# Kernel optimization log

Hardware: AMD Instinct MI355X
Metric: run time of the kernel (lower is better)

## Reference

```python
import jax, jax.numpy as jnp
import numpy as np

# --- module hyperparameters (from init_kwargs) ---
NUM_CHANNELS = 31
WINDOW_SIZE = 3
IN_DIM = 2 * WINDOW_SIZE + 1          # 7
GRID_SIZE = 5
SPLINE_ORDER = 3
GRID_RANGE = (-1.0, 1.0)
N_BASIS = GRID_SIZE + SPLINE_ORDER    # 8 spline coefficients per input dim
COEF_LEN = IN_DIM * 1 * N_BASIS       # 56
KAN_PARAMS = COEF_LEN + IN_DIM + IN_DIM  # 70 = coef + univariate_w + residual_w


def bspline_basis(x):
    """Cox-de Boor B-spline bases of order SPLINE_ORDER on a uniform grid.
    x: [...,] -> returns [..., N_BASIS]."""
    lo, hi = GRID_RANGE
    h = (hi - lo) / GRID_SIZE
    # extended knot vector: grid_size + 2*k + 1 knots
    knots = lo + h * jnp.arange(-SPLINE_ORDER, GRID_SIZE + SPLINE_ORDER + 1,
                                dtype=x.dtype)
    xe = x[..., None]
    b = ((xe >= knots[:-1]) & (xe < knots[1:])).astype(x.dtype)
    for p in range(1, SPLINE_ORDER + 1):
        left = (xe - knots[: -(p + 1)]) / (knots[p:-1] - knots[: -(p + 1)]) * b[..., :-1]
        right = (knots[p + 1:] - xe) / (knots[p + 1:] - knots[1:-p]) * b[..., 1:]
        b = left + right
    return b  # [..., N_BASIS]


def setup_inputs() -> dict:
    key = jax.random.key(0)
    k1, k2, k3 = jax.random.split(key, 3)
    B, C, D, H, W = 2, NUM_CHANNELS, IN_DIM, 192, 192
    windowed_x = jax.random.normal(k1, (B, C, D, H, W), dtype=jnp.float32)
    # hypernetwork generator: 3x3 conv  C -> KAN_PARAMS
    gen_w = jax.random.normal(k2, (KAN_PARAMS, C, 3, 3), dtype=jnp.float32) * 0.05
    gen_b = jax.random.normal(k3, (KAN_PARAMS,), dtype=jnp.float32) * 0.05
    return {"windowed_x": windowed_x, "gen_w": gen_w, "gen_b": gen_b}


def reference(windowed_x, gen_w, gen_b):
    B, C, D, H, W = windowed_x.shape
    # shared-params branch: global context -> per-pixel KAN weights
    ctx = windowed_x.mean(axis=2)  # [B, C, H, W]
    wts = jax.lax.conv_general_dilated(
        ctx, gen_w, window_strides=(1, 1), padding="SAME",
        dimension_numbers=("NCHW", "OIHW", "NCHW"))
    wts = wts + gen_b[None, :, None, None]            # [B, P, H, W]
    wts = jnp.moveaxis(wts, 1, -1)                    # [B, H, W, P]
    # unpack per-pixel KAN parameters (out_dim == 1 squeezed)
    coef = wts[..., :COEF_LEN].reshape(B, H, W, D, N_BASIS)   # [B,H,W,7,8]
    uw = wts[..., COEF_LEN:COEF_LEN + D]                      # [B,H,W,7]
    rw = wts[..., COEF_LEN + D:COEF_LEN + 2 * D]              # [B,H,W,7]
    # per-pixel, per-channel spline window evaluation (weights shared over C)
    x = jnp.moveaxis(windowed_x, 2, -1)               # [B, C, H, W, 7]
    basis = bspline_basis(x)                          # [B, C, H, W, 7, 8]
    spline = jnp.einsum("bchwdg,bhwdg,bhwd->bchw", basis, coef, uw)
    resid = jnp.einsum("bchwd,bhwd->bchw", jax.nn.silu(x), rw)
    return spline + resid                             # [B, C, H, W]
```

## Files before the change

### kernel.cpp

```cpp
#include <hip/hip_runtime.h>
#include <math.h>

#define NBATCH 2
#define NC 31
#define ND 7
#define NH 192
#define NW 192
#define HW (NH * NW)
#define NP (NBATCH * HW)
#define NBASIS 8
#define CLEN 56
#define KP 70

#define N4 (NBATCH * NC * (HW / 4))
#define GWB_N (9 * 80 * 32)

#define A_WORDS (9 * 80 * 32)
#define B_WORDS (3 * 66 * 32)

#define KPX 64

typedef __attribute__((ext_vector_type(8))) short s16x8;
typedef __attribute__((ext_vector_type(4))) float f32x4;

__device__ __forceinline__ unsigned short f2bf(float f)
{
    unsigned u = __float_as_uint(f);
    u += 0x7FFFu + ((u >> 16) & 1u);
    return (unsigned short)(u >> 16);
}

__global__ __launch_bounds__(256) void ctx_mean_kernel(
    const float4* __restrict__ x4, float4* __restrict__ ctx4,
    const float* __restrict__ gw, unsigned short* __restrict__ gwb)
{
    const int HW4 = HW / 4;
    int idx = blockIdx.x * 256 + threadIdx.x;
    if (idx < N4) {
        int hw4 = idx % HW4;
        int bc  = idx / HW4;
        const float4* src = x4 + (size_t)bc * (ND * HW4) + hw4;
        float4 a = src[0];
#pragma unroll
        for (int d = 1; d < ND; ++d) {
            float4 v = src[d * HW4];
            a.x += v.x; a.y += v.y; a.z += v.z; a.w += v.w;
        }
        const float inv = 1.0f / 7.0f;
        a.x *= inv; a.y *= inv; a.z *= inv; a.w *= inv;
        ctx4[idx] = a;
        return;
    }
    int e = idx - N4;
    if (e < GWB_N) {
        int s  = e / 2560;
        int r  = e - s * 2560;
        int m  = r >> 5;
        int ic = r & 31;
        float v = (m < KP && ic < NC) ? gw[m * (NC * 9) + ic * 9 + s] : 0.f;
        gwb[e] = f2bf(v);
    }
}

__global__ __launch_bounds__(256) void conv_kernel(
    const float* __restrict__ ctx, const unsigned short* __restrict__ gwb,
    const float* __restrict__ gb, float* __restrict__ wts)
{
    __shared__ __align__(16) unsigned short AB[A_WORDS + B_WORDS];

    const int tid  = threadIdx.x;
    const int lane = tid & 63;
    const int wv   = tid >> 6;
    const int gr   = blockIdx.x / 3;
    const int x0   = (blockIdx.x % 3) * 64;
    const int b    = gr / NH;
    const int y    = gr - b * NH;

    {
        const uint4* gs = (const uint4*)gwb;
        uint4*       gd = (uint4*)AB;
        for (int f = tid; f < A_WORDS / 8; f += 256) gd[f] = gs[f];
    }

    if (tid < 3 * 66) {
        int row = tid / 66;
        int col = tid - row * 66;
        int gy = y + row - 1, gx = x0 + col - 1;
        bool ok = (gy >= 0) && (gy < NH) && (gx >= 0) && (gx < NW);
        int cgy = ok ? gy : 0, cgx = ok ? gx : 0;
        const float* src = ctx + (size_t)(b * NC) * HW + cgy * NW + cgx;
        unsigned dw[16];
        if (ok) {
            float v[NC];
#pragma unroll
            for (int ic = 0; ic < NC; ++ic) v[ic] = src[(size_t)ic * HW];
#pragma unroll
            for (int j = 0; j < 16; ++j) {
                unsigned lo = f2bf(v[2 * j]);
                unsigned hi = (2 * j + 1 < NC) ? (unsigned)f2bf(v[2 * j + 1]) : 0u;
                dw[j] = lo | (hi << 16);
            }
        } else {
#pragma unroll
            for (int j = 0; j < 16; ++j) dw[j] = 0u;
        }
        uint4* dst = (uint4*)(AB + A_WORDS + tid * 32);
#pragma unroll
        for (int q = 0; q < 4; ++q)
            dst[q] = make_uint4(dw[4 * q], dw[4 * q + 1], dw[4 * q + 2], dw[4 * q + 3]);
    }
    __syncthreads();

    const int lm = lane & 15;
    const int kb = lane >> 4;

    f32x4 acc[5];
#pragma unroll
    for (int mt = 0; mt < 5; ++mt)
#pragma unroll
        for (int j = 0; j < 4; ++j) {
            int m = mt * 16 + kb * 4 + j;
            acc[mt][j] = (m < KP) ? gb[m] : 0.f;
        }

    const unsigned short* ap = AB + lm * 32 + kb * 8;
    const unsigned short* bp = AB + A_WORDS + (wv * 16 + lm) * 32 + kb * 8;

#pragma unroll
    for (int s = 0; s < 9; ++s) {
        const int dy = s / 3, dx = s % 3;
        s16x8 bf = *(const s16x8*)(bp + (dy * 66 + dx) * 32);
#pragma unroll
        for (int mt = 0; mt < 5; ++mt) {
            s16x8 af = *(const s16x8*)(ap + (s * 80 + mt * 16) * 32);
            acc[mt] = __builtin_amdgcn_mfma_f32_16x16x32_bf16(af, bf, acc[mt], 0, 0, 0);
        }
    }

    const int p = blockIdx.x * 64 + wv * 16 + lm;
#pragma unroll
    for (int mt = 0; mt < 5; ++mt)
#pragma unroll
        for (int j = 0; j < 4; ++j) {
            int m = mt * 16 + kb * 4 + j;
            if (m < KP) wts[(size_t)m * NP + p] = acc[mt][j];
        }
}

__device__ __forceinline__ float spline_part(float xv, const float* cb, int d)
{
    float t = __builtin_fmaf(xv, 2.5f, 5.5f);
    float fi = floorf(t);
    int i = (int)fi;
    float u = t - fi;
    float u2 = u * u, u3 = u2 * u;
    float um = 1.f - u;
    float w0 = um * um * um * (1.f / 6.f);
    float w3 = u3 * (1.f / 6.f);
    float w1 = (3.f * u3 - 6.f * u2 + 4.f) * (1.f / 6.f);
    float w2 = 1.f - w0 - w1 - w3;
    int j0 = i - 3;
    float sd = 0.f;
#pragma unroll
    for (int k = 0; k < 4; ++k) {
        int j = j0 + k;
        bool valid = ((unsigned)j) < 8u;
        int jc = j & 7;
        float wk = (k == 0) ? w0 : (k == 1) ? w1 : (k == 2) ? w2 : w3;
        float cf = cb[(d * NBASIS + jc) * KPX];
        sd += (valid ? wk : 0.f) * cf;
    }
    return sd;
}

__device__ __forceinline__ float silu(float xv)
{
    return xv / (1.f + __expf(-xv));
}

__global__ __launch_bounds__(256, 8) void kan_kernel(
    const float* __restrict__ x, const float* __restrict__ wts,
    float* __restrict__ out)
{
    __shared__ float scoef[KP * KPX];
    const int tid = threadIdx.x;
    const int p0  = blockIdx.x * KPX;

    for (int f = tid; f < KP * 32; f += 256) {
        int k = f >> 5;
        int g = f & 31;
        float2 v = *(const float2*)(wts + (size_t)k * NP + p0 + g * 2);
        *(float2*)(scoef + k * KPX + g * 2) = v;
    }
    __syncthreads();

    const int lane = tid & 63;
    const int wv   = tid >> 6;
    const int b    = p0 / HW;
    const int hw   = (p0 - b * HW) + lane;

    const float* cb = scoef + lane;

    float uw[ND], rw[ND];
#pragma unroll
    for (int d = 0; d < ND; ++d) {
        uw[d] = cb[(CLEN + d) * KPX];
        rw[d] = cb[(CLEN + ND + d) * KPX];
    }

    const int cy = blockIdx.y;
    const int c_begin = (cy == 0) ? wv * 4
                                  : ((wv == 3) ? 27 : 16 + wv * 4);

    const float* xb = x + (size_t)(b * NC) * (ND * HW) + hw;
    float* ob = out + (b * NC) * HW + hw;

    float acc[4] = {0.f, 0.f, 0.f, 0.f};
#pragma unroll
    for (int d = 0; d < ND; ++d) {
        float xv[4];
#pragma unroll
        for (int j = 0; j < 4; ++j)
            xv[j] = xb[((size_t)(c_begin + j) * ND + d) * HW];
#pragma unroll
        for (int j = 0; j < 4; ++j)
            acc[j] += uw[d] * spline_part(xv[j], cb, d) + rw[d] * silu(xv[j]);
    }
#pragma unroll
    for (int j = 0; j < 4; ++j)
        ob[(size_t)(c_begin + j) * HW] = acc[j];
}

extern "C" void kernel_launch(void* const* d_in, const int* in_sizes, int n_in,
                              void* d_out, int out_size, void* d_ws, size_t ws_size,
                              hipStream_t stream)
{
    const float* x  = (const float*)d_in[0];
    const float* gw = (const float*)d_in[1];
    const float* gb = (const float*)d_in[2];
    float* out = (float*)d_out;

    float* ctx = (float*)d_ws;
    float* wts = ctx + (size_t)NBATCH * NC * HW;
    unsigned short* gwb = (unsigned short*)d_out;

    ctx_mean_kernel<<<dim3(N4 / 256 + (GWB_N + 255) / 256), 256, 0, stream>>>(
        (const float4*)x, (float4*)ctx, gw, gwb);
    conv_kernel<<<dim3(NP / 64), 256, 0, stream>>>(ctx, gwb, gb, wts);
    kan_kernel<<<dim3(NP / KPX, 2), 256, 0, stream>>>(x, wts, out);
}
```

Before: 142.7 us.

## Fuse conv weight generation with KAN evaluation through shared memory

Merges the MFMA conv kernel and the KAN spline kernel into one kernel. The per-pixel 70 weights are written to reused LDS instead of a global wts buffer, which removes the wts write/read round trip and one launch. Each wave now handles 8 channels with software-prefetched double-buffered x loads. In exchange the grid for the KAN phase halves (no blockIdx.y split), some channels are computed redundantly (clamped at 30), and the bf16 weight staging buffer moves from the output to the workspace.

```diff
diff --git a/kernel.cpp b/kernel.cpp
--- a/kernel.cpp
+++ b/kernel.cpp
@@ -17,6 +17,7 @@
 
 #define A_WORDS (9 * 80 * 32)
 #define B_WORDS (3 * 66 * 32)
+#define SMEM_BYTES ((A_WORDS + B_WORDS) * 2)
 
 #define KPX 64
 
@@ -60,91 +61,6 @@
         float v = (m < KP && ic < NC) ? gw[m * (NC * 9) + ic * 9 + s] : 0.f;
         gwb[e] = f2bf(v);
     }
-}
-
-__global__ __launch_bounds__(256) void conv_kernel(
-    const float* __restrict__ ctx, const unsigned short* __restrict__ gwb,
-    const float* __restrict__ gb, float* __restrict__ wts)
-{
-    __shared__ __align__(16) unsigned short AB[A_WORDS + B_WORDS];
-
-    const int tid  = threadIdx.x;
-    const int lane = tid & 63;
-    const int wv   = tid >> 6;
-    const int gr   = blockIdx.x / 3;
-    const int x0   = (blockIdx.x % 3) * 64;
-    const int b    = gr / NH;
-    const int y    = gr - b * NH;
-
-    {
-        const uint4* gs = (const uint4*)gwb;
-        uint4*       gd = (uint4*)AB;
-        for (int f = tid; f < A_WORDS / 8; f += 256) gd[f] = gs[f];
-    }
-
-    if (tid < 3 * 66) {
-        int row = tid / 66;
-        int col = tid - row * 66;
-        int gy = y + row - 1, gx = x0 + col - 1;
-        bool ok = (gy >= 0) && (gy < NH) && (gx >= 0) && (gx < NW);
-        int cgy = ok ? gy : 0, cgx = ok ? gx : 0;
-        const float* src = ctx + (size_t)(b * NC) * HW + cgy * NW + cgx;
-        unsigned dw[16];
-        if (ok) {
-            float v[NC];
-#pragma unroll
-            for (int ic = 0; ic < NC; ++ic) v[ic] = src[(size_t)ic * HW];
-#pragma unroll
-            for (int j = 0; j < 16; ++j) {
-                unsigned lo = f2bf(v[2 * j]);
-                unsigned hi = (2 * j + 1 < NC) ? (unsigned)f2bf(v[2 * j + 1]) : 0u;
-                dw[j] = lo | (hi << 16);
-            }
-        } else {
-#pragma unroll
-            for (int j = 0; j < 16; ++j) dw[j] = 0u;
-        }
-        uint4* dst = (uint4*)(AB + A_WORDS + tid * 32);
-#pragma unroll
-        for (int q = 0; q < 4; ++q)
-            dst[q] = make_uint4(dw[4 * q], dw[4 * q + 1], dw[4 * q + 2], dw[4 * q + 3]);
-    }
-    __syncthreads();
-
-    const int lm = lane & 15;
-    const int kb = lane >> 4;
-
-    f32x4 acc[5];
-#pragma unroll
-    for (int mt = 0; mt < 5; ++mt)
-#pragma unroll
-        for (int j = 0; j < 4; ++j) {
-            int m = mt * 16 + kb * 4 + j;
-            acc[mt][j] = (m < KP) ? gb[m] : 0.f;
-        }
-
-    const unsigned short* ap = AB + lm * 32 + kb * 8;
-    const unsigned short* bp = AB + A_WORDS + (wv * 16 + lm) * 32 + kb * 8;
-
-#pragma unroll
-    for (int s = 0; s < 9; ++s) {
-        const int dy = s / 3, dx = s % 3;
-        s16x8 bf = *(const s16x8*)(bp + (dy * 66 + dx) * 32);
-#pragma unroll
-        for (int mt = 0; mt < 5; ++mt) {
-            s16x8 af = *(const s16x8*)(ap + (s * 80 + mt * 16) * 32);
-            acc[mt] = __builtin_amdgcn_mfma_f32_16x16x32_bf16(af, bf, acc[mt], 0, 0, 0);
-        }
-    }
-
-    const int p = blockIdx.x * 64 + wv * 16 + lm;
-#pragma unroll
-    for (int mt = 0; mt < 5; ++mt)
-#pragma unroll
-        for (int j = 0; j < 4; ++j) {
-            int m = mt * 16 + kb * 4 + j;
-            if (m < KP) wts[(size_t)m * NP + p] = acc[mt][j];
-        }
 }
 
 __device__ __forceinline__ float spline_part(float xv, const float* cb, int d)
@@ -178,57 +94,149 @@
     return xv / (1.f + __expf(-xv));
 }
 
-__global__ __launch_bounds__(256, 8) void kan_kernel(
-    const float* __restrict__ x, const float* __restrict__ wts,
+__global__ __launch_bounds__(256) void fused_kernel(
+    const float* __restrict__ ctx, const unsigned short* __restrict__ gwb,
+    const float* __restrict__ gb, const float* __restrict__ x,
     float* __restrict__ out)
 {
-    __shared__ float scoef[KP * KPX];
-    const int tid = threadIdx.x;
-    const int p0  = blockIdx.x * KPX;
-
-    for (int f = tid; f < KP * 32; f += 256) {
-        int k = f >> 5;
-        int g = f & 31;
-        float2 v = *(const float2*)(wts + (size_t)k * NP + p0 + g * 2);
-        *(float2*)(scoef + k * KPX + g * 2) = v;
-    }
-    __syncthreads();
-
+    __shared__ __align__(16) unsigned char smem[SMEM_BYTES];
+    unsigned short* A = (unsigned short*)smem;
+    unsigned short* Bt = A + A_WORDS;
+    float* scoef = (float*)smem;
+
+    const int tid  = threadIdx.x;
     const int lane = tid & 63;
     const int wv   = tid >> 6;
-    const int b    = p0 / HW;
-    const int hw   = (p0 - b * HW) + lane;
-
-    const float* cb = scoef + lane;
+    const int gr   = blockIdx.x / 3;
+    const int x0   = (blockIdx.x % 3) * 64;
+    const int b    = gr / NH;
+    const int y    = gr - b * NH;
+
+    {
+        const uint4* gs = (const uint4*)gwb;
+        uint4*       gd = (uint4*)A;
+        for (int f = tid; f < A_WORDS / 8; f += 256) gd[f] = gs[f];
+    }
+
+    if (tid < 3 * 66) {
+        int row = tid / 66;
+        int col = tid - row * 66;
+        int gy = y + row - 1, gx = x0 + col - 1;
+        bool ok = (gy >= 0) && (gy < NH) && (gx >= 0) && (gx < NW);
+        int cgy = ok ? gy : 0, cgx = ok ? gx : 0;
+        const float* src = ctx + (size_t)(b * NC) * HW + cgy * NW + cgx;
+        unsigned dw[16];
+        if (ok) {
+            float v[NC];
+#pragma unroll
+            for (int ic = 0; ic < NC; ++ic) v[ic] = src[(size_t)ic * HW];
+#pragma unroll
+            for (int j = 0; j < 16; ++j) {
+                unsigned lo = f2bf(v[2 * j]);
+                unsigned hi = (2 * j + 1 < NC) ? (unsigned)f2bf(v[2 * j + 1]) : 0u;
+                dw[j] = lo | (hi << 16);
+            }
+        } else {
+#pragma unroll
+            for (int j = 0; j < 16; ++j) dw[j] = 0u;
+        }
+        uint4* dst = (uint4*)(Bt + tid * 32);
+#pragma unroll
+        for (int q = 0; q < 4; ++q)
+            dst[q] = make_uint4(dw[4 * q], dw[4 * q + 1], dw[4 * q + 2], dw[4 * q + 3]);
+    }
+    __syncthreads();
+
+    const int lm = lane & 15;
+    const int kb = lane >> 4;
+
+    f32x4 acc[5];
+#pragma unroll
+    for (int mt = 0; mt < 5; ++mt)
+#pragma unroll
+        for (int j = 0; j < 4; ++j) {
+            int m = mt * 16 + kb * 4 + j;
+            acc[mt][j] = (m < KP) ? gb[m] : 0.f;
+        }
+
+    const unsigned short* ap = A + lm * 32 + kb * 8;
+    const unsigned short* bp = Bt + (wv * 16 + lm) * 32 + kb * 8;
+
+#pragma unroll
+    for (int s = 0; s < 9; ++s) {
+        const int dy = s / 3, dx = s % 3;
+        s16x8 bf = *(const s16x8*)(bp + (dy * 66 + dx) * 32);
+#pragma unroll
+        for (int mt = 0; mt < 5; ++mt) {
+            s16x8 af = *(const s16x8*)(ap + (s * 80 + mt * 16) * 32);
+            acc[mt] = __builtin_amdgcn_mfma_f32_16x16x32_bf16(af, bf, acc[mt], 0, 0, 0);
+        }
+    }
+    __syncthreads();
+
+    {
+        const int px = wv * 16 + lm;
+#pragma unroll
+        for (int mt = 0; mt < 5; ++mt)
+#pragma unroll
+            for (int j = 0; j < 4; ++j) {
+                int m = mt * 16 + kb * 4 + j;
+                if (m < KP) scoef[m * KPX + px] = acc[mt][j];
+            }
+    }
+    __syncthreads();
+
+    const int hw = y * NW + x0 + lane;
+    const float* cbl = scoef + lane;
 
     float uw[ND], rw[ND];
 #pragma unroll
     for (int d = 0; d < ND; ++d) {
-        uw[d] = cb[(CLEN + d) * KPX];
-        rw[d] = cb[(CLEN + ND + d) * KPX];
-    }
-
-    const int cy = blockIdx.y;
-    const int c_begin = (cy == 0) ? wv * 4
-                                  : ((wv == 3) ? 27 : 16 + wv * 4);
+        uw[d] = cbl[(CLEN + d) * KPX];
+        rw[d] = cbl[(CLEN + ND + d) * KPX];
+    }
 
     const float* xb = x + (size_t)(b * NC) * (ND * HW) + hw;
     float* ob = out + (b * NC) * HW + hw;
-
-    float acc[4] = {0.f, 0.f, 0.f, 0.f};
-#pragma unroll
-    for (int d = 0; d < ND; ++d) {
-        float xv[4];
-#pragma unroll
-        for (int j = 0; j < 4; ++j)
-            xv[j] = xb[((size_t)(c_begin + j) * ND + d) * HW];
-#pragma unroll
-        for (int j = 0; j < 4; ++j)
-            acc[j] += uw[d] * spline_part(xv[j], cb, d) + rw[d] * silu(xv[j]);
-    }
-#pragma unroll
-    for (int j = 0; j < 4; ++j)
-        ob[(size_t)(c_begin + j) * HW] = acc[j];
+    const int c0 = wv * 8;
+
+    float cur[2][ND], nxt[2][ND];
+    {
+        int ca = min(c0, 30), cb2 = min(c0 + 1, 30);
+#pragma unroll
+        for (int d = 0; d < ND; ++d) {
+            cur[0][d] = xb[((size_t)ca * ND + d) * HW];
+            cur[1][d] = xb[((size_t)cb2 * ND + d) * HW];
+        }
+    }
+
+#pragma unroll
+    for (int pr = 0; pr < 4; ++pr) {
+        int ca = min(c0 + 2 * pr, 30), cb2 = min(c0 + 2 * pr + 1, 30);
+        if (pr < 3) {
+            int na = min(c0 + 2 * pr + 2, 30), nb = min(c0 + 2 * pr + 3, 30);
+#pragma unroll
+            for (int d = 0; d < ND; ++d) {
+                nxt[0][d] = xb[((size_t)na * ND + d) * HW];
+                nxt[1][d] = xb[((size_t)nb * ND + d) * HW];
+            }
+        }
+        float sa = 0.f, sb = 0.f;
+#pragma unroll
+        for (int d = 0; d < ND; ++d) {
+            sa += uw[d] * spline_part(cur[0][d], cbl, d) + rw[d] * silu(cur[0][d]);
+            sb += uw[d] * spline_part(cur[1][d], cbl, d) + rw[d] * silu(cur[1][d]);
+        }
+        ob[(size_t)ca * HW] = sa;
+        ob[(size_t)cb2 * HW] = sb;
+        if (pr < 3) {
+#pragma unroll
+            for (int d = 0; d < ND; ++d) {
+                cur[0][d] = nxt[0][d];
+                cur[1][d] = nxt[1][d];
+            }
+        }
+    }
 }
 
 extern "C" void kernel_launch(void* const* d_in, const int* in_sizes, int n_in,
@@ -241,11 +249,9 @@
     float* out = (float*)d_out;
 
     float* ctx = (float*)d_ws;
-    float* wts = ctx + (size_t)NBATCH * NC * HW;
-    unsigned short* gwb = (unsigned short*)d_out;
+    unsigned short* gwb = (unsigned short*)(ctx + (size_t)NBATCH * NC * HW);
 
     ctx_mean_kernel<<<dim3(N4 / 256 + (GWB_N + 255) / 256), 256, 0, stream>>>(
         (const float4*)x, (float4*)ctx, gw, gwb);
-    conv_kernel<<<dim3(NP / 64), 256, 0, stream>>>(ctx, gwb, gb, wts);
-    kan_kernel<<<dim3(NP / KPX, 2), 256, 0, stream>>>(x, wts, out);
-}
+    fused_kernel<<<dim3(NP / 64), 256, 0, stream>>>(ctx, gwb, gb, x, out);
+}
```

Result: faster. 139.6 us (-2.2%).
